# Kernel optimization log

Hardware: AMD Instinct MI355X
Metric: run time of the kernel (lower is better)

Reference implementation:

```python
import jax, jax.numpy as jnp
import numpy as np

MAX_BITS = 8   # codes are stored at 8 bits (max of supported_bits), 4 codes per int32
W_BITS = 4     # active bit-width -> lut has 2**W_BITS entries per output row


def setup_inputs() -> dict:
    key = jax.random.key(0)
    k1, k2, k3 = jax.random.split(key, 3)
    B, S = 1, 2048
    OUT, IN = 8192, 8192
    x = jax.random.normal(k1, (B, S, IN), dtype=jnp.float32)
    qweight = jax.random.randint(k2, (OUT, IN // 4), 0, 2147483647, dtype=jnp.int32)
    # per-output-channel lookup table for w_bits=4 -> 16 entries
    lut = jax.random.normal(k3, (OUT, 2 ** W_BITS), dtype=jnp.float32)
    return {"x": x, "qweight": qweight, "lut": lut}


def dequant_kbit(qweight, lut, w_bits):
    # qweight: (O, K//4) int32 -> 8-bit codes (O, K)
    O = qweight.shape[0]
    shifts = jnp.array([0, 8, 16, 24], dtype=jnp.int32)
    codes = (qweight[:, :, None] >> shifts) & 0xFF          # (O, K//4, 4)
    codes = codes.reshape(O, -1)                             # (O, K)
    # any-precision: top w_bits of the 8-bit code index the w_bits LUT
    idx = codes >> (MAX_BITS - w_bits)                       # (O, K) in [0, 2**w_bits)
    weight = jnp.take_along_axis(lut, idx, axis=1)           # (O, K)
    return weight


def reference(x, qweight, lut):
    # bulk path of AnyprecisionLinear.forward (tokens > 8): dequant then matmul
    weight = dequant_kbit(qweight, lut, W_BITS)              # (O, K)
    out = jnp.einsum('bsk,ok->bso', x, weight)               # (B, S, O)
    return out
```

## Files before the change

kernel.cpp:

```cpp
#include <hip/hip_runtime.h>
#include <stdint.h>


#define M_DIM 2048
#define N_DIM 8192
#define K_DIM 8192
#define BM 256
#define BN 256
#define BK 64
#define KT (K_DIM / BK)

typedef __bf16 bf16x8 __attribute__((ext_vector_type(8)));
typedef float f32x4 __attribute__((ext_vector_type(4)));

__device__ __forceinline__ unsigned int f2bf(float f) {
  unsigned int u = __float_as_uint(f);
  return (u + 0x7FFFu + ((u >> 16) & 1u)) >> 16;
}

__global__ __launch_bounds__(256) void dequant_kernel(
    const int4* __restrict__ qw4,
    const float* __restrict__ lut,
    unsigned short* __restrict__ wb) {
  __shared__ unsigned int slut[4 * 16 * 64];
  const int wave = threadIdx.x >> 6;
  const int lane = threadIdx.x & 63;
  const int row = (blockIdx.x << 2) + wave;

  unsigned int* tbl = slut + wave * (16 * 64) + lane;
  const float* lr = lut + row * 16;
#pragma unroll
  for (int e = 0; e < 16; ++e) tbl[e * 64] = f2bf(lr[e]);

  const int4* src = qw4 + (size_t)row * 512 + lane;
  unsigned short* dst = wb + (size_t)row * K_DIM + lane * 16;

#pragma unroll
  for (int it = 0; it < 8; ++it) {
    int4 q = src[it * 64];
    unsigned int w[4] = {(unsigned int)q.x, (unsigned int)q.y,
                         (unsigned int)q.z, (unsigned int)q.w};
    unsigned int v[16];
#pragma unroll
    for (int j = 0; j < 4; ++j) {
#pragma unroll
      for (int k = 0; k < 4; ++k)
        v[j * 4 + k] = tbl[((w[j] >> (8 * k + 4)) & 15u) * 64];
    }
    uint4 o0, o1;
    o0.x = v[0] | (v[1] << 16);   o0.y = v[2]  | (v[3] << 16);
    o0.z = v[4] | (v[5] << 16);   o0.w = v[6]  | (v[7] << 16);
    o1.x = v[8] | (v[9] << 16);   o1.y = v[10] | (v[11] << 16);
    o1.z = v[12] | (v[13] << 16); o1.w = v[14] | (v[15] << 16);
    uint4* dp = (uint4*)(dst + it * 1024);
    dp[0] = o0;
    dp[1] = o1;
  }
}

__global__ __launch_bounds__(256) void cvt_x_kernel(
    const float4* __restrict__ x4, unsigned int* __restrict__ xb) {
  const int idx = blockIdx.x * 256 + threadIdx.x;
  float4 a = x4[2 * idx];
  float4 b = x4[2 * idx + 1];
  uint4 o;
  o.x = f2bf(a.x) | (f2bf(a.y) << 16);
  o.y = f2bf(a.z) | (f2bf(a.w) << 16);
  o.z = f2bf(b.x) | (f2bf(b.y) << 16);
  o.w = f2bf(b.z) | (f2bf(b.w) << 16);
  ((uint4*)xb)[idx] = o;
}


__device__ __forceinline__ void stage2(const unsigned short* __restrict__ g,
                                       unsigned short* lds, unsigned off) {
  __builtin_amdgcn_global_load_lds(
      (const __attribute__((address_space(1))) void*)(g + off),
      (__attribute__((address_space(3))) void*)lds, 16, 0, 0);
}

__device__ __forceinline__ void load_a4(const unsigned short* __restrict__ s,
                                        int row0, int aoff0, int aoff1,
                                        bf16x8 out[4][2]) {
#pragma unroll
  for (int mi = 0; mi < 4; ++mi) {
    out[mi][0] = *(const bf16x8*)(s + (row0 + mi * 16) * BK + aoff0);
    out[mi][1] = *(const bf16x8*)(s + (row0 + mi * 16) * BK + aoff1);
  }
}

__device__ __forceinline__ void load_b2(const unsigned short* __restrict__ s,
                                        int row0, int aoff0, int aoff1,
                                        bf16x8 out[2][2]) {
#pragma unroll
  for (int nj = 0; nj < 2; ++nj) {
    out[nj][0] = *(const bf16x8*)(s + (row0 + nj * 16) * BK + aoff0);
    out[nj][1] = *(const bf16x8*)(s + (row0 + nj * 16) * BK + aoff1);
  }
}

#define MFMA_Q(AF, BQ, MH, NH)                                                \
  _Pragma("unroll")                                                           \
  for (int ks = 0; ks < 2; ++ks)                                              \
    _Pragma("unroll")                                                         \
    for (int mi = 0; mi < 4; ++mi)                                            \
      _Pragma("unroll")                                                       \
      for (int nj = 0; nj < 2; ++nj)                                          \
        acc[(MH)*4 + mi][(NH)*2 + nj] =                                       \
            __builtin_amdgcn_mfma_f32_16x16x32_bf16(                          \
                AF[mi][ks], BQ[nj][ks], acc[(MH)*4 + mi][(NH)*2 + nj],        \
                0, 0, 0);

#define SBAR asm volatile("s_barrier" ::: "memory")
#define SCHEDB __builtin_amdgcn_sched_barrier(0)

#define KTILE(T, BF)                                                          \
  {                                                                           \
    const unsigned ko2 = (((T) + 2) & (KT - 1)) * BK;                         \
    const unsigned short* sa_ = sA[BF];                                       \
    const unsigned short* sb_ = sB[BF];                                       \
    const unsigned short* sa1 = sA[(BF) ^ 1];                                 \
    const unsigned short* sb1 = sB[(BF) ^ 1];                                 \
    unsigned short* waq = sA[BF] + (wave << 3) * BK;                          \
    unsigned short* wbq = sB[BF] + (wave << 3) * BK;                          \
                                \
    load_b2(sb_, bnlo + 128, aoff0, aoff1, bqB);                              \
    stage2(A, waq + 0 * BK, aU + 0u * K_DIM + ko2 + laneoff);                 \
    stage2(A, waq + 128 * BK, aU + 128u * K_DIM + ko2 + laneoff);             \
    SCHEDB;                                                                   \
    __builtin_amdgcn_s_setprio(1);                                            \
    MFMA_Q(afA, bqA, 0, 0);                                                   \
    __builtin_amdgcn_s_setprio(0);                                            \
    SCHEDB;                                                                   \
    SBAR;                                                                     \
                                \
    load_a4(sa_, wm + 64, aoff0, aoff1, afB);                                 \
    stage2(B, wbq + 0 * BK, bU + 0u * K_DIM + ko2 + laneoff);                 \
    stage2(B, wbq + 64 * BK, bU + 64u * K_DIM + ko2 + laneoff);               \
    SCHEDB;                                                                   \
    __builtin_amdgcn_s_setprio(1);                                            \
    MFMA_Q(afA, bqB, 0, 1);                                                   \
    __builtin_amdgcn_s_setprio(0);                                            \
    SCHEDB;                                                                   \
    asm volatile("s_waitcnt lgkmcnt(0)" ::: "memory");                        \
    SBAR;                                                                     \
        \
    asm volatile("s_waitcnt vmcnt(10)" ::: "memory");                         \
    load_a4(sa1, wm + 0, aoff0, aoff1, afA);                                  \
    stage2(A, waq + 64 * BK, aU + 64u * K_DIM + ko2 + laneoff);               \
    stage2(A, waq + 192 * BK, aU + 192u * K_DIM + ko2 + laneoff);             \
    SCHEDB;                                                                   \
    __builtin_amdgcn_s_setprio(1);                                            \
    MFMA_Q(afB, bqA, 1, 0);                                                   \
    __builtin_amdgcn_s_setprio(0);                                            \
    SCHEDB;                                                                   \
    SBAR;                                                                     \
        \
    asm volatile("s_waitcnt vmcnt(8)" ::: "memory");                          \
    load_b2(sb1, bnlo, aoff0, aoff1, bqA);                                    \
    stage2(B, wbq + 128 * BK, bU + 128u * K_DIM + ko2 + laneoff);             \
    stage2(B, wbq + 192 * BK, bU + 192u * K_DIM + ko2 + laneoff);             \
    SCHEDB;                                                                   \
    __builtin_amdgcn_s_setprio(1);                                            \
    MFMA_Q(afB, bqB, 1, 1);                                                   \
    __builtin_amdgcn_s_setprio(0);                                            \
    SCHEDB;                                                                   \
    asm volatile("s_waitcnt lgkmcnt(0)" ::: "memory");                        \
    asm volatile("s_waitcnt vmcnt(6)" ::: "memory");                          \
    SBAR;                                                                     \
  }

__global__ __launch_bounds__(512, 2) void gemm_bt(
    const unsigned short* __restrict__ A,
    const unsigned short* __restrict__ B,
    float* __restrict__ C) {
  __shared__ __align__(16) unsigned short sA[2][BM * BK];
  __shared__ __align__(16) unsigned short sB[2][BN * BK];

  const int tid = threadIdx.x;
  const int wave = tid >> 6;
  const int lane = tid & 63;

  const int bid = blockIdx.x;
  const int swz = (bid & 7) * 32 + (bid >> 3);
  const int m0 = (swz >> 5) * BM;
  const int n0 = (swz & 31) * BN;

  const int wm = (wave >> 2) * 128;
  const int bnlo = (wave & 3) * 32;

  const int srow = lane >> 3;
  const int scol = ((lane & 7) ^ srow) * 8;
  const unsigned laneoff = (unsigned)(srow * K_DIM + scol);
  const unsigned aU = (unsigned)((m0 + (wave << 3)) * K_DIM);
  const unsigned bU = (unsigned)((n0 + (wave << 3)) * K_DIM);

  const int rrow = lane & 15;
  const int rk = lane >> 4;
  const int aoff0 = rrow * BK + ((rk) ^ (rrow & 7)) * 8;
  const int aoff1 = rrow * BK + ((4 + rk) ^ (rrow & 7)) * 8;

  bf16x8 afA[4][2], afB[4][2];
  bf16x8 bqA[2][2], bqB[2][2];
  f32x4 acc[8][4];
#pragma unroll
  for (int m = 0; m < 8; ++m)
#pragma unroll
    for (int n = 0; n < 4; ++n)
#pragma unroll
      for (int r = 0; r < 4; ++r) acc[m][n][r] = 0.0f;

  {
    unsigned short* pa0 = sA[0] + (wave << 3) * BK;
    unsigned short* pb0 = sB[0] + (wave << 3) * BK;
    unsigned short* pa1 = sA[1] + (wave << 3) * BK;
    unsigned short* pb1 = sB[1] + (wave << 3) * BK;
    stage2(A, pa0 + 0 * BK, aU + 0u * K_DIM + laneoff);
    stage2(A, pa0 + 128 * BK, aU + 128u * K_DIM + laneoff);
    stage2(B, pb0 + 0 * BK, bU + 0u * K_DIM + laneoff);
    stage2(B, pb0 + 64 * BK, bU + 64u * K_DIM + laneoff);
    stage2(A, pa0 + 64 * BK, aU + 64u * K_DIM + laneoff);
    stage2(A, pa0 + 192 * BK, aU + 192u * K_DIM + laneoff);
    stage2(B, pb0 + 128 * BK, bU + 128u * K_DIM + laneoff);
    stage2(B, pb0 + 192 * BK, bU + 192u * K_DIM + laneoff);
    stage2(A, pa1 + 0 * BK, aU + 0u * K_DIM + BK + laneoff);
    stage2(A, pa1 + 128 * BK, aU + 128u * K_DIM + BK + laneoff);
    stage2(B, pb1 + 0 * BK, bU + 0u * K_DIM + BK + laneoff);
    stage2(B, pb1 + 64 * BK, bU + 64u * K_DIM + BK + laneoff);
    stage2(A, pa1 + 64 * BK, aU + 64u * K_DIM + BK + laneoff);
    stage2(A, pa1 + 192 * BK, aU + 192u * K_DIM + BK + laneoff);
    stage2(B, pb1 + 128 * BK, bU + 128u * K_DIM + BK + laneoff);
    stage2(B, pb1 + 192 * BK, bU + 192u * K_DIM + BK + laneoff);
  }
  asm volatile("s_waitcnt vmcnt(8)" ::: "memory");
  SBAR;
  load_a4(sA[0], wm + 0, aoff0, aoff1, afA);
  load_b2(sB[0], bnlo, aoff0, aoff1, bqA);
  asm volatile("s_waitcnt lgkmcnt(0)" ::: "memory");
  SBAR;

#pragma unroll 1
  for (int tt = 0; tt < KT / 2; ++tt) {
    KTILE(2 * tt, 0)
    KTILE(2 * tt + 1, 1)
  }
  asm volatile("s_waitcnt vmcnt(0) lgkmcnt(0)" ::: "memory");

  const int crow0 = m0 + wm + 4 * rk;
  const int ccol0 = n0 + bnlo + rrow;
#pragma unroll
  for (int m = 0; m < 8; ++m)
#pragma unroll
    for (int n = 0; n < 4; ++n)
#pragma unroll
      for (int r = 0; r < 4; ++r)
        C[(size_t)(crow0 + m * 16 + r) * N_DIM + ccol0 + (n >> 1) * 128 +
          (n & 1) * 16] = acc[m][n][r];
}

__global__ void naive_kernel(const float* __restrict__ x,
                             const int* __restrict__ qw,
                             const float* __restrict__ lut,
                             float* __restrict__ out) {
  int o = blockIdx.x * blockDim.x + threadIdx.x;
  int s = blockIdx.y;
  const float* xr = x + (size_t)s * K_DIM;
  const unsigned int* qr = (const unsigned int*)qw + (size_t)o * (K_DIM / 4);
  const float* l = lut + o * 16;
  float acc = 0.f;
  for (int w = 0; w < K_DIM / 4; ++w) {
    unsigned int q = qr[w];
    acc += xr[w * 4 + 0] * l[(q >> 4) & 15u]
         + xr[w * 4 + 1] * l[(q >> 12) & 15u]
         + xr[w * 4 + 2] * l[(q >> 20) & 15u]
         + xr[w * 4 + 3] * l[(q >> 28) & 15u];
  }
  out[(size_t)s * N_DIM + o] = acc;
}

extern "C" void kernel_launch(void* const* d_in, const int* in_sizes, int n_in,
                              void* d_out, int out_size, void* d_ws,
                              size_t ws_size, hipStream_t stream) {
  const float* x = (const float*)d_in[0];
  const int* qw = (const int*)d_in[1];
  const float* lut = (const float*)d_in[2];
  float* out = (float*)d_out;

  const size_t wb_elems = (size_t)N_DIM * K_DIM;
  const size_t xb_elems = (size_t)M_DIM * K_DIM;
  const size_t need = (wb_elems + xb_elems) * sizeof(unsigned short);

  if (ws_size >= need) {
    unsigned short* wb = (unsigned short*)d_ws;
    unsigned short* xb = wb + wb_elems;

    hipLaunchKernelGGL(dequant_kernel, dim3(N_DIM / 4), dim3(256), 0, stream,
                       (const int4*)qw, lut, wb);

    const int n_thr = M_DIM * K_DIM / 8;
    hipLaunchKernelGGL(cvt_x_kernel, dim3(n_thr / 256), dim3(256), 0, stream,
                       (const float4*)x, (unsigned int*)xb);

    hipLaunchKernelGGL(gemm_bt, dim3((M_DIM / BM) * (N_DIM / BN)), dim3(512),
                       0, stream, xb, wb, out);
  } else {
    dim3 grid(N_DIM / 256, M_DIM);
    hipLaunchKernelGGL(naive_kernel, grid, dim3(256), 0, stream, x, qw, lut,
                       out);
  }
}
```

Before: 461.7 us.

## Fuse LUT dequantization of weights into the GEMM mainloop

Drops the separate dequant kernel and its full bf16 weight buffer. Each GEMM block now loads packed 8-bit codes directly, looks them up in a per-block shared-memory bf16 LUT, and writes the swizzled B tile into LDS for the next K step. The pipeline is also simplified to one K-tile lookahead with a full vmcnt/lgkmcnt(0) wait per tile. This removes the weight write/read round trip through HBM, at the cost of ALU/LDS lookup work inside the mainloop, lost overlap, and dequantizing every weight row once per M-block.

```diff
diff --git a/kernel.cpp b/kernel.cpp
--- a/kernel.cpp
+++ b/kernel.cpp
@@ -9,6 +9,7 @@
 #define BN 256
 #define BK 64
 #define KT (K_DIM / BK)
+#define LUTS 17
 
 typedef __bf16 bf16x8 __attribute__((ext_vector_type(8)));
 typedef float f32x4 __attribute__((ext_vector_type(4)));
@@ -16,46 +17,6 @@
 __device__ __forceinline__ unsigned int f2bf(float f) {
   unsigned int u = __float_as_uint(f);
   return (u + 0x7FFFu + ((u >> 16) & 1u)) >> 16;
-}
-
-__global__ __launch_bounds__(256) void dequant_kernel(
-    const int4* __restrict__ qw4,
-    const float* __restrict__ lut,
-    unsigned short* __restrict__ wb) {
-  __shared__ unsigned int slut[4 * 16 * 64];
-  const int wave = threadIdx.x >> 6;
-  const int lane = threadIdx.x & 63;
-  const int row = (blockIdx.x << 2) + wave;
-
-  unsigned int* tbl = slut + wave * (16 * 64) + lane;
-  const float* lr = lut + row * 16;
-#pragma unroll
-  for (int e = 0; e < 16; ++e) tbl[e * 64] = f2bf(lr[e]);
-
-  const int4* src = qw4 + (size_t)row * 512 + lane;
-  unsigned short* dst = wb + (size_t)row * K_DIM + lane * 16;
-
-#pragma unroll
-  for (int it = 0; it < 8; ++it) {
-    int4 q = src[it * 64];
-    unsigned int w[4] = {(unsigned int)q.x, (unsigned int)q.y,
-                         (unsigned int)q.z, (unsigned int)q.w};
-    unsigned int v[16];
-#pragma unroll
-    for (int j = 0; j < 4; ++j) {
-#pragma unroll
-      for (int k = 0; k < 4; ++k)
-        v[j * 4 + k] = tbl[((w[j] >> (8 * k + 4)) & 15u) * 64];
-    }
-    uint4 o0, o1;
-    o0.x = v[0] | (v[1] << 16);   o0.y = v[2]  | (v[3] << 16);
-    o0.z = v[4] | (v[5] << 16);   o0.w = v[6]  | (v[7] << 16);
-    o1.x = v[8] | (v[9] << 16);   o1.y = v[10] | (v[11] << 16);
-    o1.z = v[12] | (v[13] << 16); o1.w = v[14] | (v[15] << 16);
-    uint4* dp = (uint4*)(dst + it * 1024);
-    dp[0] = o0;
-    dp[1] = o1;
-  }
 }
 
 __global__ __launch_bounds__(256) void cvt_x_kernel(
@@ -114,68 +75,71 @@
 #define SBAR asm volatile("s_barrier" ::: "memory")
 #define SCHEDB __builtin_amdgcn_sched_barrier(0)
 
-#define KTILE(T, BF)                                                          \
+#define BCHUNK(W0, W1, J)                                                     \
   {                                                                           \
-    const unsigned ko2 = (((T) + 2) & (KT - 1)) * BK;                         \
-    const unsigned short* sa_ = sA[BF];                                       \
-    const unsigned short* sb_ = sB[BF];                                       \
-    const unsigned short* sa1 = sA[(BF) ^ 1];                                 \
-    const unsigned short* sb1 = sB[(BF) ^ 1];                                 \
-    unsigned short* waq = sA[BF] + (wave << 3) * BK;                          \
-    unsigned short* wbq = sB[BF] + (wave << 3) * BK;                          \
-                                \
-    load_b2(sb_, bnlo + 128, aoff0, aoff1, bqB);                              \
-    stage2(A, waq + 0 * BK, aU + 0u * K_DIM + ko2 + laneoff);                 \
-    stage2(A, waq + 128 * BK, aU + 128u * K_DIM + ko2 + laneoff);             \
-    SCHEDB;                                                                   \
+    unsigned v0 = slut_row[((W0) >> 4) & 15u];                                \
+    unsigned v1 = slut_row[((W0) >> 12) & 15u];                               \
+    unsigned v2 = slut_row[((W0) >> 20) & 15u];                               \
+    unsigned v3 = slut_row[(W0) >> 28];                                       \
+    unsigned v4 = slut_row[((W1) >> 4) & 15u];                                \
+    unsigned v5 = slut_row[((W1) >> 12) & 15u];                               \
+    unsigned v6 = slut_row[((W1) >> 20) & 15u];                               \
+    unsigned v7 = slut_row[(W1) >> 28];                                       \
+    uint4 o;                                                                  \
+    o.x = v0 | (v1 << 16);                                                    \
+    o.y = v2 | (v3 << 16);                                                    \
+    o.z = v4 | (v5 << 16);                                                    \
+    o.w = v6 | (v7 << 16);                                                    \
+    *(uint4*)(bw + ((((bkh << 2) + (J)) ^ bsw) << 3)) = o;                    \
+  }
+
+#define BDEQ(Q0, Q1, BW)                                                      \
+  {                                                                           \
+    unsigned short* bw = BW;                                                  \
+    BCHUNK((unsigned)(Q0).x, (unsigned)(Q0).y, 0)                             \
+    BCHUNK((unsigned)(Q0).z, (unsigned)(Q0).w, 1)                             \
+    BCHUNK((unsigned)(Q1).x, (unsigned)(Q1).y, 2)                             \
+    BCHUNK((unsigned)(Q1).z, (unsigned)(Q1).w, 3)                             \
+  }
+
+#define FTILE(T, P)                                                           \
+  {                                                                           \
+    const unsigned ko1 = (((T) + 1) & (KT - 1)) * BK;                         \
+    uint4 q0 = qwrow[ko1 >> 4];                                               \
+    uint4 q1 = qwrow[(ko1 >> 4) + 1];                                         \
+    unsigned short* nxtA = sA[(P) ^ 1] + (wave << 3) * BK;                    \
+    stage2(A, nxtA + 0 * BK, aU + 0u * K_DIM + ko1 + laneoff);                \
+    stage2(A, nxtA + 64 * BK, aU + 64u * K_DIM + ko1 + laneoff);              \
+    stage2(A, nxtA + 128 * BK, aU + 128u * K_DIM + ko1 + laneoff);            \
+    stage2(A, nxtA + 192 * BK, aU + 192u * K_DIM + ko1 + laneoff);            \
+    const unsigned short* sa_ = sA[P];                                        \
+    const unsigned short* sb_ = sB[P];                                        \
+    load_b2(sb_, bnlo, aoff0, aoff1, bq0);                                    \
+    load_b2(sb_, bnlo + 128, aoff0, aoff1, bq1);                              \
+    load_a4(sa_, wm, aoff0, aoff1, af);                                       \
     __builtin_amdgcn_s_setprio(1);                                            \
-    MFMA_Q(afA, bqA, 0, 0);                                                   \
+    MFMA_Q(af, bq0, 0, 0);                                                    \
+    MFMA_Q(af, bq1, 0, 1);                                                    \
+    __builtin_amdgcn_s_setprio(0);                                            \
+    load_a4(sa_, wm + 64, aoff0, aoff1, af);                                  \
+    __builtin_amdgcn_s_setprio(1);                                            \
+    MFMA_Q(af, bq0, 1, 0);                                                    \
+    MFMA_Q(af, bq1, 1, 1);                                                    \
     __builtin_amdgcn_s_setprio(0);                                            \
     SCHEDB;                                                                   \
+    BDEQ(q0, q1, sB[(P) ^ 1] + brow * BK)                                     \
+    asm volatile("s_waitcnt vmcnt(0) lgkmcnt(0)" ::: "memory");               \
     SBAR;                                                                     \
-                                \
-    load_a4(sa_, wm + 64, aoff0, aoff1, afB);                                 \
-    stage2(B, wbq + 0 * BK, bU + 0u * K_DIM + ko2 + laneoff);                 \
-    stage2(B, wbq + 64 * BK, bU + 64u * K_DIM + ko2 + laneoff);               \
-    SCHEDB;                                                                   \
-    __builtin_amdgcn_s_setprio(1);                                            \
-    MFMA_Q(afA, bqB, 0, 1);                                                   \
-    __builtin_amdgcn_s_setprio(0);                                            \
-    SCHEDB;                                                                   \
-    asm volatile("s_waitcnt lgkmcnt(0)" ::: "memory");                        \
-    SBAR;                                                                     \
-        \
-    asm volatile("s_waitcnt vmcnt(10)" ::: "memory");                         \
-    load_a4(sa1, wm + 0, aoff0, aoff1, afA);                                  \
-    stage2(A, waq + 64 * BK, aU + 64u * K_DIM + ko2 + laneoff);               \
-    stage2(A, waq + 192 * BK, aU + 192u * K_DIM + ko2 + laneoff);             \
-    SCHEDB;                                                                   \
-    __builtin_amdgcn_s_setprio(1);                                            \
-    MFMA_Q(afB, bqA, 1, 0);                                                   \
-    __builtin_amdgcn_s_setprio(0);                                            \
-    SCHEDB;                                                                   \
-    SBAR;                                                                     \
-        \
-    asm volatile("s_waitcnt vmcnt(8)" ::: "memory");                          \
-    load_b2(sb1, bnlo, aoff0, aoff1, bqA);                                    \
-    stage2(B, wbq + 128 * BK, bU + 128u * K_DIM + ko2 + laneoff);             \
-    stage2(B, wbq + 192 * BK, bU + 192u * K_DIM + ko2 + laneoff);             \
-    SCHEDB;                                                                   \
-    __builtin_amdgcn_s_setprio(1);                                            \
-    MFMA_Q(afB, bqB, 1, 1);                                                   \
-    __builtin_amdgcn_s_setprio(0);                                            \
-    SCHEDB;                                                                   \
-    asm volatile("s_waitcnt lgkmcnt(0)" ::: "memory");                        \
-    asm volatile("s_waitcnt vmcnt(6)" ::: "memory");                          \
-    SBAR;                                                                     \
-  }
-
-__global__ __launch_bounds__(512, 2) void gemm_bt(
+  }
+
+__global__ __launch_bounds__(512, 2) void gemm_fused(
     const unsigned short* __restrict__ A,
-    const unsigned short* __restrict__ B,
+    const uint4* __restrict__ qw4,
+    const float* __restrict__ lut,
     float* __restrict__ C) {
   __shared__ __align__(16) unsigned short sA[2][BM * BK];
   __shared__ __align__(16) unsigned short sB[2][BN * BK];
+  __shared__ unsigned slut[256 * LUTS];
 
   const int tid = threadIdx.x;
   const int wave = tid >> 6;
@@ -193,15 +157,20 @@
   const int scol = ((lane & 7) ^ srow) * 8;
   const unsigned laneoff = (unsigned)(srow * K_DIM + scol);
   const unsigned aU = (unsigned)((m0 + (wave << 3)) * K_DIM);
-  const unsigned bU = (unsigned)((n0 + (wave << 3)) * K_DIM);
+
+  const int brow = (wave << 5) + (lane >> 1);
+  const int bkh = lane & 1;
+  const int bsw = brow & 7;
+  const unsigned* slut_row = slut + brow * LUTS;
+  const uint4* qwrow = qw4 + (size_t)(n0 + brow) * 512 + bkh * 2;
 
   const int rrow = lane & 15;
   const int rk = lane >> 4;
   const int aoff0 = rrow * BK + ((rk) ^ (rrow & 7)) * 8;
   const int aoff1 = rrow * BK + ((4 + rk) ^ (rrow & 7)) * 8;
 
-  bf16x8 afA[4][2], afB[4][2];
-  bf16x8 bqA[2][2], bqB[2][2];
+  bf16x8 af[4][2];
+  bf16x8 bq0[2][2], bq1[2][2];
   f32x4 acc[8][4];
 #pragma unroll
   for (int m = 0; m < 8; ++m)
@@ -210,41 +179,32 @@
 #pragma unroll
       for (int r = 0; r < 4; ++r) acc[m][n][r] = 0.0f;
 
+  {
+    const float* lr = lut + (size_t)(n0 + (tid >> 1)) * 16 + (tid & 1) * 8;
+    unsigned* dst = slut + (tid >> 1) * LUTS + (tid & 1) * 8;
+#pragma unroll
+    for (int e = 0; e < 8; ++e) dst[e] = f2bf(lr[e]);
+  }
+
+  uint4 p0 = qwrow[0];
+  uint4 p1 = qwrow[1];
   {
     unsigned short* pa0 = sA[0] + (wave << 3) * BK;
-    unsigned short* pb0 = sB[0] + (wave << 3) * BK;
-    unsigned short* pa1 = sA[1] + (wave << 3) * BK;
-    unsigned short* pb1 = sB[1] + (wave << 3) * BK;
     stage2(A, pa0 + 0 * BK, aU + 0u * K_DIM + laneoff);
+    stage2(A, pa0 + 64 * BK, aU + 64u * K_DIM + laneoff);
     stage2(A, pa0 + 128 * BK, aU + 128u * K_DIM + laneoff);
-    stage2(B, pb0 + 0 * BK, bU + 0u * K_DIM + laneoff);
-    stage2(B, pb0 + 64 * BK, bU + 64u * K_DIM + laneoff);
-    stage2(A, pa0 + 64 * BK, aU + 64u * K_DIM + laneoff);
     stage2(A, pa0 + 192 * BK, aU + 192u * K_DIM + laneoff);
-    stage2(B, pb0 + 128 * BK, bU + 128u * K_DIM + laneoff);
-    stage2(B, pb0 + 192 * BK, bU + 192u * K_DIM + laneoff);
-    stage2(A, pa1 + 0 * BK, aU + 0u * K_DIM + BK + laneoff);
-    stage2(A, pa1 + 128 * BK, aU + 128u * K_DIM + BK + laneoff);
-    stage2(B, pb1 + 0 * BK, bU + 0u * K_DIM + BK + laneoff);
-    stage2(B, pb1 + 64 * BK, bU + 64u * K_DIM + BK + laneoff);
-    stage2(A, pa1 + 64 * BK, aU + 64u * K_DIM + BK + laneoff);
-    stage2(A, pa1 + 192 * BK, aU + 192u * K_DIM + BK + laneoff);
-    stage2(B, pb1 + 128 * BK, bU + 128u * K_DIM + BK + laneoff);
-    stage2(B, pb1 + 192 * BK, bU + 192u * K_DIM + BK + laneoff);
-  }
-  asm volatile("s_waitcnt vmcnt(8)" ::: "memory");
-  SBAR;
-  load_a4(sA[0], wm + 0, aoff0, aoff1, afA);
-  load_b2(sB[0], bnlo, aoff0, aoff1, bqA);
-  asm volatile("s_waitcnt lgkmcnt(0)" ::: "memory");
+  }
+  __syncthreads();
+  BDEQ(p0, p1, sB[0] + brow * BK)
+  asm volatile("s_waitcnt vmcnt(0) lgkmcnt(0)" ::: "memory");
   SBAR;
 
 #pragma unroll 1
   for (int tt = 0; tt < KT / 2; ++tt) {
-    KTILE(2 * tt, 0)
-    KTILE(2 * tt + 1, 1)
-  }
-  asm volatile("s_waitcnt vmcnt(0) lgkmcnt(0)" ::: "memory");
+    FTILE(2 * tt, 0)
+    FTILE(2 * tt + 1, 1)
+  }
 
   const int crow0 = m0 + wm + 4 * rk;
   const int ccol0 = n0 + bnlo + rrow;
@@ -286,23 +246,18 @@
   const float* lut = (const float*)d_in[2];
   float* out = (float*)d_out;
 
-  const size_t wb_elems = (size_t)N_DIM * K_DIM;
   const size_t xb_elems = (size_t)M_DIM * K_DIM;
-  const size_t need = (wb_elems + xb_elems) * sizeof(unsigned short);
+  const size_t need = xb_elems * sizeof(unsigned short);
 
   if (ws_size >= need) {
-    unsigned short* wb = (unsigned short*)d_ws;
-    unsigned short* xb = wb + wb_elems;
-
-    hipLaunchKernelGGL(dequant_kernel, dim3(N_DIM / 4), dim3(256), 0, stream,
-                       (const int4*)qw, lut, wb);
+    unsigned short* xb = (unsigned short*)d_ws;
 
     const int n_thr = M_DIM * K_DIM / 8;
     hipLaunchKernelGGL(cvt_x_kernel, dim3(n_thr / 256), dim3(256), 0, stream,
                        (const float4*)x, (unsigned int*)xb);
 
-    hipLaunchKernelGGL(gemm_bt, dim3((M_DIM / BM) * (N_DIM / BN)), dim3(512),
-                       0, stream, xb, wb, out);
+    hipLaunchKernelGGL(gemm_fused, dim3((M_DIM / BM) * (N_DIM / BN)),
+                       dim3(512), 0, stream, xb, (const uint4*)qw, lut, out);
   } else {
     dim3 grid(N_DIM / 256, M_DIM);
     hipLaunchKernelGGL(naive_kernel, grid, dim3(256), 0, stream, x, qw, lut,
```

Result: faster. 433.1 us (-6.2%).
